# Optimization experiments

Hardware: AMD Instinct MI355X
Metric: run time of the kernel (lower is better)

The kernel has to match this reference:

```python
import jax, jax.numpy as jnp
import numpy as np


def setup_inputs() -> dict:
    key = jax.random.key(0)
    k1, k2, k3, k4 = jax.random.split(key, 4)
    B, H, L, D = 2, 16, 2048, 128
    q = jax.random.normal(k1, (B, H, L, D), dtype=jnp.float32)
    k = jax.random.normal(k2, (B, H, L, D), dtype=jnp.float32)
    v = jax.random.normal(k3, (B, H, L, D), dtype=jnp.float32)
    query = jax.random.normal(k4, (B, H, L, D), dtype=jnp.float32)
    padding_mask = jnp.zeros((B, H, L, 1), dtype=bool)
    return {"q": q, "k": k, "v": v, "query": query,
            "padding_mask": padding_mask, "dropout_p": 0}


def reference(q, k, v, query, padding_mask, dropout_p):
    # qk = q @ k^T  -> [B,H,Lq,Lk]
    qk = jnp.einsum('bhqd,bhkd->bhqk', q, k)
    # NOTE: faithful to source -- scores are MULTIPLIED by sqrt(D), not divided.
    scale = jnp.asarray(np.sqrt(np.float32(q.shape[-1])), dtype=q.dtype)
    attn = jax.nn.softmax(qk * scale, axis=-1)
    # dropout_p is a static Python int (0 here) -> dropout is identity.
    if dropout_p:
        keep = jax.random.bernoulli(jax.random.key(1), 1.0 - dropout_p, attn.shape)
        attn = jnp.where(keep, attn / (1.0 - dropout_p), 0.0)
    out = jnp.einsum('bhqk,bhkd->bhqd', attn, v)
    # post-mask with the closed-over `query` tensor, then cast to int64
    out = jnp.where(padding_mask, query, out).astype(jnp.int64)
    return out
```

## Files before the change

kernel.cpp:

```cpp
#include <hip/hip_runtime.h>
#include <math.h>


#define KL 2048
#define KD 128
#define TQ 32
#define CAPS 96
#define CAPF 40
#define QP 132
#define GEMMQ 384
#define SCALEF 0x1.6A09E6p+3f
#define CUTU 4.35f

#define KH_ELEMS  (2 * 16 * KL * KD)
#define NROWS     (2 * 16 * KL)

typedef __attribute__((ext_vector_type(8))) short bf16x8;
typedef __attribute__((ext_vector_type(4))) float f32x4;

static __device__ __forceinline__ unsigned short f2bf(float f) {
    unsigned u = __float_as_uint(f);
    return (unsigned short)((u + 0x7FFFu + ((u >> 16) & 1u)) >> 16);
}

static __device__ __forceinline__ unsigned fkey(float f) {
    const unsigned u = __float_as_uint(f);
    return u ^ ((unsigned)((int)u >> 31) | 0x80000000u);
}
static __device__ __forceinline__ float funkey(unsigned k) {
    return __uint_as_float(k ^ ((unsigned)(~((int)k >> 31)) | 0x80000000u));
}

__global__ void __launch_bounds__(256)
cvt_k_bf16(const float* __restrict__ kp, unsigned short* __restrict__ kh) {
    const int i4 = (blockIdx.x * 256 + threadIdx.x) * 4;
    const float4 v = *(const float4*)(kp + i4);
    ushort4 h; h.x = f2bf(v.x); h.y = f2bf(v.y); h.z = f2bf(v.z); h.w = f2bf(v.w);
    *(ushort4*)(kh + i4) = h;
}

__global__ void __launch_bounds__(256)
attn_screen(const float* __restrict__ qp, const unsigned short* __restrict__ kh,
            int* __restrict__ gcnt, unsigned short* __restrict__ gcand)
{
    __shared__ unsigned       rmaxI[TQ];
    __shared__ int            cnt[TQ];
    __shared__ unsigned short candK[TQ * CAPS];
    __shared__ float          candS[TQ * CAPS];

    const int tid  = threadIdx.x;
    const int lane = tid & 63;
    const int wave = tid >> 6;
    const int l15  = lane & 15;
    const int quad = lane >> 4;

    const int lin = blockIdx.y * (KL / TQ) + blockIdx.x;
    const int nl  = (lin & 7) * 256 + (lin >> 3);
    const int bh  = nl >> 6;
    const int q0  = (nl & 63) * TQ;

    const size_t base  = (size_t)bh * (KL * KD);
    const size_t baseh = (size_t)bh * KL * KD;

    if (tid < TQ) { cnt[tid] = 0; rmaxI[tid] = 0x00800000u;  }

    bf16x8 aA[2][4];
    #pragma unroll
    for (int a = 0; a < 2; ++a)
        #pragma unroll
        for (int s = 0; s < 4; ++s) {
            const int row = q0 + a * 16 + l15;
            const int d0 = s * 32 + quad * 8;
            const float4 x = *(const float4*)(qp + base + (size_t)row * KD + d0);
            const float4 y = *(const float4*)(qp + base + (size_t)row * KD + d0 + 4);
            bf16x8 af;
            af[0] = (short)f2bf(x.x); af[1] = (short)f2bf(x.y);
            af[2] = (short)f2bf(x.z); af[3] = (short)f2bf(x.w);
            af[4] = (short)f2bf(y.x); af[5] = (short)f2bf(y.y);
            af[6] = (short)f2bf(y.z); af[7] = (short)f2bf(y.w);
            aA[a][s] = af;
        }
    __syncthreads();

    float rmaxL[8];
    float thrR[8];
    #pragma unroll
    for (int i = 0; i < 8; ++i) rmaxL[i] = -3.4e38f;

    const unsigned short* kwbase =
        kh + baseh + (size_t)(16 * wave + l15) * KD + quad * 8;

    #pragma unroll 1
    for (int tp = 0; tp < 2; ++tp) {
        const unsigned short* kb = kwbase + (size_t)tp * 64 * KD;
        const bf16x8 b0 = *(const bf16x8*)(kb + 0);
        const bf16x8 b1 = *(const bf16x8*)(kb + 32);
        const bf16x8 b2 = *(const bf16x8*)(kb + 64);
        const bf16x8 b3 = *(const bf16x8*)(kb + 96);
        f32x4 ac0 = {0.f,0.f,0.f,0.f}, ac1 = {0.f,0.f,0.f,0.f};
        ac0 = __builtin_amdgcn_mfma_f32_16x16x32_bf16(aA[0][0], b0, ac0, 0,0,0);
        ac1 = __builtin_amdgcn_mfma_f32_16x16x32_bf16(aA[1][0], b0, ac1, 0,0,0);
        ac0 = __builtin_amdgcn_mfma_f32_16x16x32_bf16(aA[0][1], b1, ac0, 0,0,0);
        ac1 = __builtin_amdgcn_mfma_f32_16x16x32_bf16(aA[1][1], b1, ac1, 0,0,0);
        ac0 = __builtin_amdgcn_mfma_f32_16x16x32_bf16(aA[0][2], b2, ac0, 0,0,0);
        ac1 = __builtin_amdgcn_mfma_f32_16x16x32_bf16(aA[1][2], b2, ac1, 0,0,0);
        ac0 = __builtin_amdgcn_mfma_f32_16x16x32_bf16(aA[0][3], b3, ac0, 0,0,0);
        ac1 = __builtin_amdgcn_mfma_f32_16x16x32_bf16(aA[1][3], b3, ac1, 0,0,0);
        #pragma unroll
        for (int a = 0; a < 2; ++a)
            #pragma unroll
            for (int g = 0; g < 4; ++g)
                rmaxL[a * 4 + g] = fmaxf(rmaxL[a * 4 + g],
                                         (a == 0) ? ac0[g] : ac1[g]);
    }
    #pragma unroll
    for (int a = 0; a < 2; ++a)
        #pragma unroll
        for (int g = 0; g < 4; ++g) {
            float vv = rmaxL[a * 4 + g];
            vv = fmaxf(vv, __shfl_xor(vv, 1, 64));
            vv = fmaxf(vv, __shfl_xor(vv, 2, 64));
            vv = fmaxf(vv, __shfl_xor(vv, 4, 64));
            vv = fmaxf(vv, __shfl_xor(vv, 8, 64));
            rmaxL[a * 4 + g] = vv;
            if (l15 == 0) atomicMax(&rmaxI[a * 16 + quad * 4 + g], fkey(vv));
        }
    __syncthreads();
    #pragma unroll
    for (int a = 0; a < 2; ++a)
        #pragma unroll
        for (int g = 0; g < 4; ++g)
            thrR[a * 4 + g] = funkey(__hip_atomic_load(
                    &rmaxI[a * 16 + quad * 4 + g],
                    __ATOMIC_RELAXED, __HIP_MEMORY_SCOPE_WORKGROUP)) - CUTU;

    bf16x8 cur0 = *(const bf16x8*)(kwbase + 0);
    bf16x8 cur1 = *(const bf16x8*)(kwbase + 32);
    bf16x8 cur2 = *(const bf16x8*)(kwbase + 64);
    bf16x8 cur3 = *(const bf16x8*)(kwbase + 96);

    #pragma unroll 1
    for (int t = 0; t < KL / 64; ++t) {
        const int tn = (t < KL / 64 - 1) ? t + 1 : t;
        const unsigned short* kbn = kwbase + (size_t)tn * 64 * KD;
        const bf16x8 nx0 = *(const bf16x8*)(kbn + 0);
        const bf16x8 nx1 = *(const bf16x8*)(kbn + 32);
        const bf16x8 nx2 = *(const bf16x8*)(kbn + 64);
        const bf16x8 nx3 = *(const bf16x8*)(kbn + 96);

        f32x4 ac0 = {0.f,0.f,0.f,0.f}, ac1 = {0.f,0.f,0.f,0.f};
        __builtin_amdgcn_s_setprio(1);
        ac0 = __builtin_amdgcn_mfma_f32_16x16x32_bf16(aA[0][0], cur0, ac0, 0,0,0);
        ac1 = __builtin_amdgcn_mfma_f32_16x16x32_bf16(aA[1][0], cur0, ac1, 0,0,0);
        ac0 = __builtin_amdgcn_mfma_f32_16x16x32_bf16(aA[0][1], cur1, ac0, 0,0,0);
        ac1 = __builtin_amdgcn_mfma_f32_16x16x32_bf16(aA[1][1], cur1, ac1, 0,0,0);
        ac0 = __builtin_amdgcn_mfma_f32_16x16x32_bf16(aA[0][2], cur2, ac0, 0,0,0);
        ac1 = __builtin_amdgcn_mfma_f32_16x16x32_bf16(aA[1][2], cur2, ac1, 0,0,0);
        ac0 = __builtin_amdgcn_mfma_f32_16x16x32_bf16(aA[0][3], cur3, ac0, 0,0,0);
        ac1 = __builtin_amdgcn_mfma_f32_16x16x32_bf16(aA[1][3], cur3, ac1, 0,0,0);
        __builtin_amdgcn_s_setprio(0);

        #pragma unroll
        for (int a = 0; a < 2; ++a)
            #pragma unroll
            for (int g = 0; g < 4; ++g) {
                const int j = a * 4 + g;
                const float sc = (a == 0) ? ac0[g] : ac1[g];
                rmaxL[j] = fmaxf(rmaxL[j], sc);
                const bool pred = sc > thrR[j];
                const unsigned long long mask = __ballot(pred);
                const unsigned mq = (unsigned)(mask >> (16 * quad)) & 0xFFFFu;
                if (mq) {
                    const int row = a * 16 + quad * 4 + g;
                    int basec = 0;
                    if (l15 == 0) basec = atomicAdd(&cnt[row], __popc(mq));
                    basec = __shfl(basec, lane & 48, 64);
                    if (pred) {
                        const int idx = basec + __popc(mq & ((1u << l15) - 1u));
                        if (idx < CAPS) {
                            candK[row * CAPS + idx] =
                                (unsigned short)(t * 64 + 16 * wave + l15);
                            candS[row * CAPS + idx] = sc;
                        }
                    }
                }
            }

        if ((t & 3) == 3) {
            #pragma unroll
            for (int a = 0; a < 2; ++a)
                #pragma unroll
                for (int g = 0; g < 4; ++g) {
                    float vv = rmaxL[a * 4 + g];
                    vv = fmaxf(vv, __shfl_xor(vv, 1, 64));
                    vv = fmaxf(vv, __shfl_xor(vv, 2, 64));
                    vv = fmaxf(vv, __shfl_xor(vv, 4, 64));
                    vv = fmaxf(vv, __shfl_xor(vv, 8, 64));
                    rmaxL[a * 4 + g] = vv;
                    if (l15 == 0)
                        atomicMax(&rmaxI[a * 16 + quad * 4 + g], fkey(vv));
                }
            #pragma unroll
            for (int a = 0; a < 2; ++a)
                #pragma unroll
                for (int g = 0; g < 4; ++g)
                    thrR[a * 4 + g] = funkey(__hip_atomic_load(
                            &rmaxI[a * 16 + quad * 4 + g],
                            __ATOMIC_RELAXED, __HIP_MEMORY_SCOPE_WORKGROUP)) - CUTU;
        }
        cur0 = nx0; cur1 = nx1; cur2 = nx2; cur3 = nx3;
    }
    __syncthreads();

    if (tid < TQ) {
        const float rm = funkey(rmaxI[tid]);
        const float thr = rm - CUTU;
        const int n0 = min(cnt[tid], CAPS);
        unsigned short* ck = &candK[tid * CAPS];
        float* cs = &candS[tid * CAPS];
        int m = 0;
        for (int i = 0; i < n0; ++i)
            if (cs[i] > thr) ck[m++] = ck[i];
        if (m > CAPF) m = CAPF;
        for (int i = 1; i < m; ++i) {
            const unsigned short key = ck[i];
            int j = i - 1;
            while (j >= 0 && ck[j] > key) { ck[j + 1] = ck[j]; --j; }
            ck[j + 1] = key;
        }
        const int grow = bh * KL + q0 + tid;
        gcnt[grow] = m;
        unsigned short* gc = gcand + (size_t)grow * CAPF;
        for (int i = 0; i < m; ++i) gc[i] = ck[i];
    }
}

__global__ void __launch_bounds__(256)
attn_finish(const float* __restrict__ qp, const float* __restrict__ kp,
            const float* __restrict__ vp, const float* __restrict__ queryp,
            const unsigned char* __restrict__ maskp,
            const int* __restrict__ gcnt, const unsigned short* __restrict__ gcand,
            int* __restrict__ outp)
{
#pragma clang fp contract(off)
    __shared__ float          Qs[TQ * QP];
    __shared__ int            cntA[TQ];
    __shared__ unsigned short candK[TQ * CAPF];
    __shared__ float          candS[TQ * CAPF];
    __shared__ float          candA[TQ * CAPF];

    const int tid = threadIdx.x;

    const int lin = blockIdx.y * (KL / TQ) + blockIdx.x;
    const int nl  = (lin & 7) * 256 + (lin >> 3);
    const int bh  = nl >> 6;
    const int q0  = (nl & 63) * TQ;

    const size_t base = (size_t)bh * (KL * KD);
    const int rowbase = bh * KL + q0;

    #pragma unroll
    for (int i = 0; i < 4; ++i) {
        const int idx = tid + i * 256, r = idx >> 5, c4 = (idx & 31) << 2;
        *(float4*)&Qs[r * QP + c4] =
            *(const float4*)(qp + base + (size_t)(q0 + r) * KD + c4);
    }
    {
        const unsigned short* gc = gcand + (size_t)rowbase * CAPF;
        #pragma unroll
        for (int i = 0; i < (TQ * CAPF + 255) / 256; ++i) {
            const int idx = tid + i * 256;
            if (idx < TQ * CAPF) candK[idx] = gc[idx];
        }
        if (tid < TQ) cntA[tid] = gcnt[rowbase + tid];
    }
    __syncthreads();

    {
        const int r = tid >> 3, j = tid & 7;
        const int n = cntA[r];
        const float* qrow = &Qs[r * QP];
        for (int i = j; i < n; i += 8) {
            const int kk = candK[r * CAPF + i];
            const float* krow = kp + base + (size_t)kk * KD;
            float s = 0.f;
            #pragma unroll 8
            for (int d = 0; d < KD; d += 4) {
                const float4 kv = *(const float4*)(krow + d);
                const float4 qv = *(const float4*)(qrow + d);
                s = fmaf(qv.x, kv.x, s);
                s = fmaf(qv.y, kv.y, s);
                s = fmaf(qv.z, kv.z, s);
                s = fmaf(qv.w, kv.w, s);
            }
            candS[r * CAPF + i] = s * SCALEF;
        }
    }
    __syncthreads();

    if (tid < TQ) {
        const int r = tid, n = cntA[r];
        float m = -3.4e38f;
        for (int i = 0; i < n; ++i) m = fmaxf(m, candS[r * CAPF + i]);
        for (int i = 0; i < n; ++i) {
            const float dm = candS[r * CAPF + i] - m;
            candA[r * CAPF + i] = (float)exp((double)dm);
        }
        float* E = &Qs[r * 129];
        float leaves[16];
        int p = 0;
        #pragma unroll 1
        for (int b = 0; b < 16; ++b) {
            const int pstart = p;
            while (p < n && (candK[r * CAPF + p] >> 7) == b) ++p;
            const int cb = p - pstart;
            float leaf = 0.0f;
            if (cb == 1) {
                leaf = candA[r * CAPF + pstart];
            } else if (cb >= 2) {
                for (int jj = 0; jj < 128; ++jj) E[jj] = 0.0f;
                for (int jj = pstart; jj < p; ++jj)
                    E[candK[r * CAPF + jj] & 127] = candA[r * CAPF + jj];
                float R[16];
                for (int l = 0; l < 16; ++l)
                    R[l] = ((E[l] + E[16 + l]) + (E[32 + l] + E[48 + l]))
                         + ((E[64 + l] + E[80 + l]) + (E[96 + l] + E[112 + l]));
                for (int l = 0; l < 8; ++l) R[l] = R[l] + R[l + 8];
                for (int l = 0; l < 4; ++l) R[l] = R[l] + R[l + 4];
                R[0] = R[0] + R[2]; R[1] = R[1] + R[3];
                leaf = R[0] + R[1];
            }
            leaves[b] = leaf;
        }
        float t2[8], t3[4];
        for (int jj = 0; jj < 8; ++jj) t2[jj] = leaves[2 * jj] + leaves[2 * jj + 1];
        for (int jj = 0; jj < 4; ++jj) t3[jj] = t2[2 * jj] + t2[2 * jj + 1];
        const float sig = (t3[0] + t3[1]) + (t3[2] + t3[3]);
        for (int i = 0; i < n; ++i)
            candA[r * CAPF + i] = candA[r * CAPF + i] / sig;
    }
    __syncthreads();

    for (int rr = 0; rr < TQ; rr += 2) {
        const int r = rr + (tid >> 7);
        const int d = tid & 127;
        const int n = cntA[r];
        float o = 0.0f, part = 0.0f;
        int cprev = 0;
        #pragma unroll 1
        for (int i0 = 0; i0 < n; i0 += 8) {
            float pa[8], pv[8]; int pc[8];
            #pragma unroll
            for (int u = 0; u < 8; ++u) {
                const int ix = i0 + u;
                const bool act = ix < n;
                const int kk = act ? (int)candK[r * CAPF + ix] : 0;
                pa[u] = act ? candA[r * CAPF + ix] : 0.0f;
                pc[u] = act ? ((kk * 683) >> 18) : 0;
                pv[u] = act ? vp[base + (size_t)kk * KD + d] : 0.0f;
            }
            #pragma unroll
            for (int u = 0; u < 8; ++u) {
                if (i0 + u < n) {
                    if (pc[u] != cprev) { o = o + part; part = 0.0f; cprev = pc[u]; }
                    part = fmaf(pa[u], pv[u], part);
                }
            }
        }
        o = o + part;
        int res = (int)o;
        const int grow = q0 + r;
        if (maskp[(size_t)bh * KL + grow])
            res = (int)queryp[base + (size_t)grow * KD + d];
        outp[base + (size_t)grow * KD + d] = res;
    }
}

extern "C" void kernel_launch(void* const* d_in, const int* in_sizes, int n_in,
                              void* d_out, int out_size, void* d_ws, size_t ws_size,
                              hipStream_t stream) {
    const float* q     = (const float*)d_in[0];
    const float* k     = (const float*)d_in[1];
    const float* v     = (const float*)d_in[2];
    const float* query = (const float*)d_in[3];
    const unsigned char* mask = (const unsigned char*)d_in[4];
    int* out = (int*)d_out;

    unsigned short* kh    = (unsigned short*)d_ws;
    int*            gcnt  = (int*)((char*)d_ws + (size_t)KH_ELEMS * 2);
    unsigned short* gcand = (unsigned short*)((char*)d_ws + (size_t)KH_ELEMS * 2
                                              + (size_t)NROWS * 4);

    cvt_k_bf16<<<dim3(8192), dim3(256), 0, stream>>>(k, kh);

    dim3 grid(KL / TQ, 32, 1);
    dim3 block(256, 1, 1);
    attn_screen<<<grid, block, 0, stream>>>(q, kh, gcnt, gcand);
    attn_finish<<<grid, block, 0, stream>>>(q, k, v, query, mask, gcnt, gcand, out);
}
```

Measured before the change: 439.9 us.

## Parallelize softmax exp/normalize across threads and simplify candidate append

The finish kernel's per-row softmax no longer runs on only 32 threads. Each row's double-precision exp and its normalization divide are now spread over 8 threads, using shared rowM/rowSig and extra barriers. A two-candidate block is summed directly instead of through the 128-entry zero-fill tree. In the score kernel, the ballot/popc aggregated LDS append is replaced by a per-lane atomicAdd, which simplifies control flow but may add LDS atomic contention and changes the order of candidate slots.

```diff
diff --git a/kernel.cpp b/kernel.cpp
--- a/kernel.cpp
+++ b/kernel.cpp
@@ -167,21 +167,13 @@
                 const int j = a * 4 + g;
                 const float sc = (a == 0) ? ac0[g] : ac1[g];
                 rmaxL[j] = fmaxf(rmaxL[j], sc);
-                const bool pred = sc > thrR[j];
-                const unsigned long long mask = __ballot(pred);
-                const unsigned mq = (unsigned)(mask >> (16 * quad)) & 0xFFFFu;
-                if (mq) {
+                if (sc > thrR[j]) {
                     const int row = a * 16 + quad * 4 + g;
-                    int basec = 0;
-                    if (l15 == 0) basec = atomicAdd(&cnt[row], __popc(mq));
-                    basec = __shfl(basec, lane & 48, 64);
-                    if (pred) {
-                        const int idx = basec + __popc(mq & ((1u << l15) - 1u));
-                        if (idx < CAPS) {
-                            candK[row * CAPS + idx] =
-                                (unsigned short)(t * 64 + 16 * wave + l15);
-                            candS[row * CAPS + idx] = sc;
-                        }
+                    const int idx = atomicAdd(&cnt[row], 1);
+                    if (idx < CAPS) {
+                        candK[row * CAPS + idx] =
+                            (unsigned short)(t * 64 + 16 * wave + l15);
+                        candS[row * CAPS + idx] = sc;
                     }
                 }
             }
@@ -248,6 +240,8 @@
     __shared__ unsigned short candK[TQ * CAPF];
     __shared__ float          candS[TQ * CAPF];
     __shared__ float          candA[TQ * CAPF];
+    __shared__ float          rowM[TQ];
+    __shared__ float          rowSig[TQ];
 
     const int tid = threadIdx.x;
 
@@ -299,13 +293,26 @@
     __syncthreads();
 
     if (tid < TQ) {
-        const int r = tid, n = cntA[r];
+        const int n = cntA[tid];
         float m = -3.4e38f;
-        for (int i = 0; i < n; ++i) m = fmaxf(m, candS[r * CAPF + i]);
-        for (int i = 0; i < n; ++i) {
+        for (int i = 0; i < n; ++i) m = fmaxf(m, candS[tid * CAPF + i]);
+        rowM[tid] = m;
+    }
+    __syncthreads();
+
+    {
+        const int r = tid >> 3, j = tid & 7;
+        const int n = cntA[r];
+        const float m = rowM[r];
+        for (int i = j; i < n; i += 8) {
             const float dm = candS[r * CAPF + i] - m;
             candA[r * CAPF + i] = (float)exp((double)dm);
         }
+    }
+    __syncthreads();
+
+    if (tid < TQ) {
+        const int r = tid, n = cntA[r];
         float* E = &Qs[r * 129];
         float leaves[16];
         int p = 0;
@@ -317,7 +324,9 @@
             float leaf = 0.0f;
             if (cb == 1) {
                 leaf = candA[r * CAPF + pstart];
-            } else if (cb >= 2) {
+            } else if (cb == 2) {
+                leaf = candA[r * CAPF + pstart] + candA[r * CAPF + pstart + 1];
+            } else if (cb >= 3) {
                 for (int jj = 0; jj < 128; ++jj) E[jj] = 0.0f;
                 for (int jj = pstart; jj < p; ++jj)
                     E[candK[r * CAPF + jj] & 127] = candA[r * CAPF + jj];
@@ -335,8 +344,15 @@
         float t2[8], t3[4];
         for (int jj = 0; jj < 8; ++jj) t2[jj] = leaves[2 * jj] + leaves[2 * jj + 1];
         for (int jj = 0; jj < 4; ++jj) t3[jj] = t2[2 * jj] + t2[2 * jj + 1];
-        const float sig = (t3[0] + t3[1]) + (t3[2] + t3[3]);
-        for (int i = 0; i < n; ++i)
+        rowSig[r] = (t3[0] + t3[1]) + (t3[2] + t3[3]);
+    }
+    __syncthreads();
+
+    {
+        const int r = tid >> 3, j = tid & 7;
+        const int n = cntA[r];
+        const float sig = rowSig[r];
+        for (int i = j; i < n; i += 8)
             candA[r * CAPF + i] = candA[r * CAPF + i] / sig;
     }
     __syncthreads();
```

After: 412.9 us. 6.1% less time.
